# Kernel optimization log

Measured on AMD Instinct MI355X. Metric: run time of the kernel, lower is better.

## Reference

```python
import jax, jax.numpy as jnp
import numpy as np

A_DIM = 18
HID = 512
LSTM_IN = HID + A_DIM + 1  # 531


def setup_inputs() -> dict:
    key = jax.random.key(0)
    ks = jax.random.split(key, 26)
    T, B = 80, 64
    inp = {}
    inp["o"] = jax.random.randint(ks[0], (T, B, 1, 84, 84), 0, 255, dtype=jnp.int32)
    inp["a"] = jax.random.randint(ks[1], (T, B), 0, A_DIM, dtype=jnp.int32)
    inp["r"] = jax.random.normal(ks[2], (T, B), dtype=jnp.float32)
    inp["done"] = jax.random.randint(ks[3], (T, B), 0, 2, dtype=jnp.int32)
    inp["h0"] = jnp.zeros((B, HID), dtype=jnp.float32)
    inp["c0"] = jnp.zeros((B, HID), dtype=jnp.float32)

    def gw(k, shape, s=0.05):
        return (jax.random.normal(k, shape, dtype=jnp.float32) * s)

    # CNN trunk params (torch Conv2d OIHW layout)
    inp["conv1_w"] = gw(ks[4], (32, 1, 8, 8))
    inp["conv1_b"] = jnp.zeros((32,), jnp.float32)
    inp["conv2_w"] = gw(ks[5], (64, 32, 4, 4))
    inp["conv2_b"] = jnp.zeros((64,), jnp.float32)
    inp["conv3_w"] = gw(ks[6], (64, 64, 3, 3))
    inp["conv3_b"] = jnp.zeros((64,), jnp.float32)
    inp["fc_w"] = gw(ks[7], (HID, 64 * 7 * 7))
    inp["fc_b"] = jnp.zeros((HID,), jnp.float32)
    # LSTM params (torch gate order: i, f, g, o)
    inp["W_ih"] = gw(ks[8], (4 * HID, LSTM_IN))
    inp["W_hh"] = gw(ks[9], (4 * HID, HID))
    inp["b_ih"] = jnp.zeros((4 * HID,), jnp.float32)
    inp["b_hh"] = jnp.zeros((4 * HID,), jnp.float32)
    # Dueling heads
    inp["adv_w1"] = gw(ks[10], (HID, HID))
    inp["adv_b1"] = jnp.zeros((HID,), jnp.float32)
    inp["adv_w2"] = gw(ks[11], (A_DIM, HID))
    inp["adv_b2"] = jnp.zeros((A_DIM,), jnp.float32)
    inp["val_w1"] = gw(ks[12], (HID, HID))
    inp["val_b1"] = jnp.zeros((HID,), jnp.float32)
    inp["val_w2"] = gw(ks[13], (1, HID))
    inp["val_b2"] = jnp.zeros((1,), jnp.float32)
    return inp


def _conv(x, w, b, stride):
    y = jax.lax.conv_general_dilated(
        x, w, (stride, stride), 'VALID',
        dimension_numbers=('NCHW', 'OIHW', 'NCHW'))
    return y + b[None, :, None, None]


def reference(o, a, r, done, h0, c0,
              conv1_w, conv1_b, conv2_w, conv2_b, conv3_w, conv3_b,
              fc_w, fc_b, W_ih, W_hh, b_ih, b_hh,
              adv_w1, adv_b1, adv_w2, adv_b2,
              val_w1, val_b1, val_w2, val_b2):
    T, B = o.shape[0], o.shape[1]
    x = o.reshape(T * B, 1, 84, 84).astype(jnp.float32) / 255.0
    x = jax.nn.relu(_conv(x, conv1_w, conv1_b, 4))   # [TB,32,20,20]
    x = jax.nn.relu(_conv(x, conv2_w, conv2_b, 2))   # [TB,64,9,9]
    x = jax.nn.relu(_conv(x, conv3_w, conv3_b, 1))   # [TB,64,7,7]
    x = x.reshape(T * B, 64 * 7 * 7)
    hidden = jax.nn.relu(x @ fc_w.T + fc_b).reshape(T, B, HID)

    a_one_hot = jax.nn.one_hot(a, A_DIM, dtype=jnp.float32)      # [T,B,A]
    lstm_in = jnp.concatenate([hidden, r[..., None], a_one_hot], axis=-1)  # [T,B,531]
    keep = (1.0 - done.astype(jnp.float32))[..., None]           # [T,B,1]
    bias = b_ih + b_hh

    def step(carry, inp_t):
        h, c = carry
        x_t, m = inp_t
        h = h * m
        c = c * m
        g = x_t @ W_ih.T + h @ W_hh.T + bias   # [B, 4H]
        i, f, gg, oo = jnp.split(g, 4, axis=-1)
        c = jax.nn.sigmoid(f) * c + jax.nn.sigmoid(i) * jnp.tanh(gg)
        h = jax.nn.sigmoid(oo) * jnp.tanh(c)
        return (h, c), h

    (hT, cT), hs = jax.lax.scan(step, (h0, c0), (lstm_in, keep))
    z = hs.reshape(T * B, HID)

    adv = jax.nn.relu(z @ adv_w1.T + adv_b1) @ adv_w2.T + adv_b2  # [TB,A]
    val = jax.nn.relu(z @ val_w1.T + val_b1) @ val_w2.T + val_b2  # [TB,1]
    q = val + (adv - adv.mean(axis=1, keepdims=True))
    return q.reshape(T, B, A_DIM), hT, cT
```

## Files before the change

### kernel.cpp

```cpp
#include <hip/hip_runtime.h>
#include <hip/hip_bf16.h>
#include <stdint.h>

typedef __bf16 bf16;
typedef __bf16 bfrag __attribute__((ext_vector_type(8)));
typedef short s16x8 __attribute__((ext_vector_type(8)));
typedef float f32x4 __attribute__((ext_vector_type(4)));
typedef float f32x16 __attribute__((ext_vector_type(16)));
typedef uint32_t u32x4 __attribute__((ext_vector_type(4)));

#define DEV __device__ __forceinline__

DEV bfrag ldg16(const bf16* p){ return *(const bfrag*)p; }

struct U64x2 { uint64_t a, b; };
DEV bfrag ld2x8(const bf16* p){
  U64x2 t; t.a = *(const uint64_t*)p; t.b = *(const uint64_t*)(p+4);
  return __builtin_bit_cast(bfrag, t);
}
DEV bfrag ld4x4(const char* p){
  u32x4 t;
  t[0] = *(const uint32_t*)p;
  t[1] = *(const uint32_t*)(p+4);
  t[2] = *(const uint32_t*)(p+8);
  t[3] = *(const uint32_t*)(p+12);
  return __builtin_bit_cast(bfrag, t);
}

DEV f32x4  mfma16(bfrag a, bfrag b, f32x4  c){ return __builtin_amdgcn_mfma_f32_16x16x32_bf16(a,b,c,0,0,0); }
DEV f32x16 mfma32(bfrag a, bfrag b, f32x16 c){ return __builtin_amdgcn_mfma_f32_32x32x16_bf16(a,b,c,0,0,0); }

DEV f32x16 zero16(){
  f32x16 v;
  for(int i=0;i<16;++i) v[i]=0.f;
  return v;
}
DEV f32x4 zero4(){
  f32x4 v;
  for(int i=0;i<4;++i) v[i]=0.f;
  return v;
}

DEV float sigm(float x){ return 1.0f/(1.0f+__expf(-x)); }
DEV float ftanh(float x){ float e = __expf(2.f*x); return 1.f - 2.f/(e+1.f); }

DEV u32x4 ldcg4(const uint32_t* p){
  u32x4 r;
  asm volatile("global_load_dwordx4 %0, %1, off sc0 sc1" : "=v"(r) : "v"(p));
  return r;
}

DEV uint32_t pk2f(float a, float b){
  bf16 x = (bf16)a, y = (bf16)b;
  return (uint32_t)__builtin_bit_cast(uint16_t,x) | ((uint32_t)__builtin_bit_cast(uint16_t,y)<<16);
}

DEV void gl_lds16(const bf16* g, void* l){
  __builtin_amdgcn_global_load_lds(
      (const __attribute__((address_space(1))) uint32_t*)g,
      (__attribute__((address_space(3))) uint32_t*)l, 16, 0, 0);
}

__global__ __launch_bounds__(256) void k_prep(
    const float* __restrict__ c1w, const float* __restrict__ c2w,
    const float* __restrict__ c3w, const float* __restrict__ fcw,
    const float* __restrict__ Wih, const float* __restrict__ WhhF,
    const float* __restrict__ bih, const float* __restrict__ bhh,
    const float* __restrict__ aw1, const float* __restrict__ aw2,
    const float* __restrict__ vw1, const float* __restrict__ vw2,
    const float* __restrict__ h0, const float* __restrict__ ab1,
    const float* __restrict__ vb1,
    bf16* w1b, bf16* w2r, bf16* w3r, bf16* fcwr, bf16* Wx, bf16* Whh,
    float* biasL, float* Wr, float* Wa, bf16* headw1, float* headb1,
    bf16* w2cat, uint32_t* hcurT)
{
  long i = (long)blockIdx.x*256 + threadIdx.x;
  if (i < 2048){ int co=(int)(i>>6), k=(int)(i&63);
    w1b[i] = (bf16)(c1w[co*64+k]*(1.f/255.f)); return; } i -= 2048;
  if (i < 32768){ int o=(int)(i>>9), k=(int)(i&511);
    int ky=k>>7, kx=(k>>5)&3, ci=k&31;
    w2r[i] = (bf16)c2w[((o*32+ci)*4+ky)*4+kx]; return; } i -= 32768;
  if (i < 36864){ int o=(int)(i/576), k=(int)(i%576);
    int ky=k/192, rem=k-ky*192, kx=rem>>6, ci=rem&63;
    w3r[i] = (bf16)c3w[((o*64+ci)*3+ky)*3+kx]; return; } i -= 36864;
  if (i < 1605632){
    int o=(int)(i/3136), rem=(int)(i%3136);
    int ci=rem/49, yx=rem-ci*49, y=yx/7, x=yx-y*7;
    fcwr[o*3200 + y*448 + x*64 + ci] = (bf16)fcw[i]; return; } i -= 1605632;
  if (i < 32768){ int o=(int)(i>>6), k=(int)(i&63);
    fcwr[o*3200 + 3136 + k] = (bf16)0.f; return; } i -= 32768;
  if (i < 1048576){ int n=(int)(i>>9), k=(int)(i&511);
    Wx[i] = (bf16)Wih[n*531+k]; return; } i -= 1048576;
  if (i < 1048576){ int n=(int)(i>>9), k=(int)(i&511);
    Whh[i] = (bf16)WhhF[n*512+k]; return; } i -= 1048576;
  if (i < 2048){ biasL[i] = bih[i]+bhh[i]; return; } i -= 2048;
  if (i < 2048){ Wr[i] = Wih[i*531+512]; return; } i -= 2048;
  if (i < 36864){ int j=(int)(i>>11), n=(int)(i&2047);
    Wa[i] = Wih[n*531+513+j]; return; } i -= 36864;
  if (i < 524288){ headw1[i] = (bf16)(i<262144 ? aw1[i] : vw1[i-262144]); return; } i -= 524288;
  if (i < 1024){ headb1[i] = (i<512) ? ab1[i] : vb1[i-512]; return; } i -= 1024;
  if (i < 32768){ int n=(int)(i>>10), k=(int)(i&1023);
    float v = 0.f;
    if (n<18 && k<512) v = aw2[n*512+k];
    else if (n==18 && k>=512) v = vw2[k-512];
    w2cat[i] = (bf16)v; return; } i -= 32768;
  if (i < 32768){
    if (i < 16384){
      int row = (int)(i>>8), wd = (int)(i&255);
      uint32_t pk = pk2f(h0[row*512 + wd*2], h0[row*512 + wd*2 + 1]);
      hcurT[i] = pk & ~0x00010001u;
    } else {
      hcurT[i] = 0x00010000u;
    }
    return;
  }
}

__global__ __launch_bounds__(256,2) void k_conv12(
    const int* __restrict__ o, const bf16* __restrict__ w1b,
    const float* __restrict__ c1b, const bf16* __restrict__ w2r,
    const float* __restrict__ c2b, bf16* __restrict__ act2)
{
  __shared__ bf16 lact[2][15200];
  const int tid = threadIdx.x;
  const int w = tid>>6, l = tid&63;
  const int img = w>>1, h = w&1;
  const long gimg = (long)blockIdx.x*2 + img;
  const int* ip = o + gimg*7056;
  char* lw = (char*)&lact[img][0];
  {
    bfrag bw[4];
    #pragma unroll
    for (int ks=0;ks<4;++ks) bw[ks] = ldg16(w1b + (l&31)*64 + ks*16 + 8*(l>>5));
    const float bias = c1b[l&31];
    for (int mt=h; mt<13; mt+=2){
      f32x16 acc = zero16();
      int m0 = mt*32 + (l&31);
      int p  = m0>399 ? 399 : m0;
      int oy = p/20, ox = p - oy*20;
      #pragma unroll
      for (int ks=0;ks<4;++ks){
        int ky = 2*ks + (l>>5);
        const int* q = ip + (oy*4+ky)*84 + ox*4;
        int4 i0 = *(const int4*)q;
        int4 i1 = *(const int4*)(q+4);
        bfrag a;
        a[0]=(bf16)(float)i0.x; a[1]=(bf16)(float)i0.y;
        a[2]=(bf16)(float)i0.z; a[3]=(bf16)(float)i0.w;
        a[4]=(bf16)(float)i1.x; a[5]=(bf16)(float)i1.y;
        a[6]=(bf16)(float)i1.z; a[7]=(bf16)(float)i1.w;
        acc = mfma32(a, bw[ks], acc);
      }
      #pragma unroll
      for (int r2=0;r2<16;++r2){
        int row = (r2&3) + 8*(r2>>2) + 4*(l>>5);
        int m = mt*32 + row;
        if (m < 400){
          float v = acc[r2] + bias; v = v>0.f ? v : 0.f;
          *(bf16*)(lw + m*76 + (l&31)*2) = (bf16)v;
        }
      }
    }
  }
  __syncthreads();
  {
    f32x16 acc2[3];
    #pragma unroll
    for (int a2=0;a2<3;++a2) acc2[a2]=zero16();
    int pb[3];
    #pragma unroll
    for (int mt=0;mt<3;++mt){
      int m = mt*32 + (l&31); int p = m>80 ? 80 : m;
      int oy = p/9, ox = p - oy*9;
      pb[mt] = (oy*2)*20 + ox*2;
    }
    #pragma unroll 4
    for (int ks=0; ks<32; ++ks){
      int k  = ks*16 + 8*(l>>5);
      int ky = k>>7, kx = (k>>5)&3, ci = k&31;
      bfrag b0 = ldg16(w2r + (32*h + (l&31))*512 + k);
      #pragma unroll
      for (int mt=0; mt<3; ++mt){
        int p2 = pb[mt] + ky*20 + kx;
        bfrag a = ld4x4(lw + p2*76 + ci*2);
        acc2[mt] = mfma32(a, b0, acc2[mt]);
      }
    }
    const float bias2 = c2b[32*h + (l&31)];
    #pragma unroll
    for (int mt=0; mt<3; ++mt){
      #pragma unroll
      for (int r2=0;r2<16;++r2){
        int row = (r2&3) + 8*(r2>>2) + 4*(l>>5);
        int m = mt*32 + row;
        if (m < 81){
          float v = acc2[mt][r2] + bias2; v = v>0.f ? v : 0.f;
          act2[gimg*5184 + m*64 + 32*h + (l&31)] = (bf16)v;
        }
      }
    }
  }
}

__global__ __launch_bounds__(256,2) void k_conv3(
    const bf16* __restrict__ act2, const bf16* __restrict__ w3r,
    const float* __restrict__ c3b, bf16* __restrict__ act3)
{
  const int tid=threadIdx.x, w=tid>>6, l=tid&63;
  const long img = (long)blockIdx.x*4 + w;
  const bf16* A = act2 + img*5184;
  f32x16 acc[2][2];
  #pragma unroll
  for(int a2=0;a2<2;++a2){ acc[a2][0]=zero16(); acc[a2][1]=zero16(); }
  #pragma unroll 4
  for (int ks=0; ks<36; ++ks){
    int k  = ks*16 + 8*(l>>5);
    int ky = k/192, rem = k - ky*192, kx = rem>>6, ci = rem&63;
    bfrag b0 = ldg16(w3r + (l&31)*576 + k);
    bfrag b1 = ldg16(w3r + (32+(l&31))*576 + k);
    #pragma unroll
    for (int mt=0; mt<2; ++mt){
      int m = mt*32 + (l&31); int p = m>48 ? 48 : m;
      int oy = p/7, ox = p - oy*7;
      bfrag a = ldg16(A + ((oy+ky)*9 + (ox+kx))*64 + ci);
      acc[mt][0] = mfma32(a, b0, acc[mt][0]);
      acc[mt][1] = mfma32(a, b1, acc[mt][1]);
    }
  }
  const float bias0 = c3b[l&31], bias1 = c3b[32+(l&31)];
  #pragma unroll
  for (int mt=0; mt<2; ++mt){
    #pragma unroll
    for (int r2=0;r2<16;++r2){
      int row = (r2&3) + 8*(r2>>2) + 4*(l>>5);
      int m = mt*32 + row;
      if (m < 50){
        float v0 = 0.f, v1 = 0.f;
        if (m < 49){
          v0 = acc[mt][0][r2] + bias0; v0 = v0>0.f ? v0 : 0.f;
          v1 = acc[mt][1][r2] + bias1; v1 = v1>0.f ? v1 : 0.f;
        }
        act3[img*3200 + m*64 + (l&31)]      = (bf16)v0;
        act3[img*3200 + m*64 + 32 + (l&31)] = (bf16)v1;
      }
    }
  }
}

template<bool RELU, bool OUTBF16>
__global__ __launch_bounds__(256,4) void k_gemm(
    const bf16* __restrict__ A, long lda,
    const bf16* __restrict__ W, long ldb,
    const float* __restrict__ bias,
    float* __restrict__ outF, bf16* __restrict__ outB, long ldo, int K,
    const float* __restrict__ fixR, const int* __restrict__ fixA,
    const float* __restrict__ fixWr, const float* __restrict__ fixWa)
{
  __shared__ bf16 sA[8192];
  char* sb = (char*)sA;
  const int tid=threadIdx.x, w=tid>>6, l=tid&63;
  const int m0 = blockIdx.x*64, n0 = blockIdx.y*128;
  f32x16 acc[2]; acc[0]=zero16(); acc[1]=zero16();
  const int mt = w&1;
  const int rowa = mt*32 + (l&31);
  for (int kc=0; kc<K; kc+=128){
    __syncthreads();
    #pragma unroll
    for (int j=0;j<4;++j){
      int idx = j*64 + l;
      int row = w*16 + (idx>>4);
      int seg = idx&15;
      const bf16* gp = A + (long)(m0+row)*lda + kc + (((seg*16) ^ ((row&15)<<4))>>1);
      gl_lds16(gp, sb + w*4096 + j*1024);
    }
    asm volatile("s_waitcnt vmcnt(0)" ::: "memory");
    __syncthreads();
    #pragma unroll
    for (int ks=0; ks<8; ++ks){
      bfrag a = *(const bfrag*)(sb + rowa*256 + ((ks*32 + (l>>5)*16) ^ ((rowa&15)<<4)));
      #pragma unroll
      for (int j=0;j<2;++j){
        int nt = (w>>1)*2 + j;
        bfrag b = ldg16(W + (long)(n0 + nt*32 + (l&31))*ldb + kc + ks*16 + 8*(l>>5));
        acc[j] = mfma32(a, b, acc[j]);
      }
    }
  }
  #pragma unroll
  for (int j=0;j<2;++j){
    int nt = (w>>1)*2 + j;
    int gc = n0 + nt*32 + (l&31);
    float bv = bias ? bias[gc] : 0.f;
    float wrv = fixR ? fixWr[gc] : 0.f;
    #pragma unroll
    for (int r2=0;r2<16;++r2){
      int row = (r2&3) + 8*(r2>>2) + 4*(l>>5);
      long gr = m0 + mt*32 + row;
      float v = acc[j][r2] + bv;
      if (fixR) v += fixR[gr]*wrv + fixWa[(long)fixA[gr]*2048 + gc];
      if (RELU) v = v>0.f ? v : 0.f;
      if (OUTBF16) outB[gr*ldo + gc] = (bf16)v;
      else         outF[gr*ldo + gc] = v;
    }
  }
}

__global__ __launch_bounds__(256,1) void k_lstm(
    const bf16* __restrict__ G, const int* __restrict__ done,
    const float* __restrict__ c0, const bf16* __restrict__ Whh,
    uint32_t* __restrict__ hcurT, bf16* __restrict__ hseq,
    float* __restrict__ outH, float* __restrict__ outC)
{
  __shared__ bf16 sh2[8192];
  __shared__ float sg[4][16][33];
  __shared__ float sc[16][33];
  __shared__ char  sdone[80][16];
  const int tid=threadIdx.x, w=tid>>6, l=tid&63;
  const int blk=blockIdx.x;
  const int grp=(blk&7)>>1, jj=((blk&1)<<3)|(blk>>3);
  const int bb = grp*16, uu = jj*32;

  for (int p=tid; p<512; p+=256){ int m=p>>5, u=p&31; sc[m][u] = c0[(bb+m)*512 + uu + u]; }
  for (int p=tid; p<1280; p+=256){ int t=p>>4, m=p&15; sdone[t][m] = (char)done[t*64 + bb + m]; }

  bfrag wb0[16], wb1[16];
  {
    const long row0 = (long)w*512 + uu + (l&15);
    #pragma unroll
    for (int ks=0; ks<16; ++ks){
      int k = ks*32 + 8*(l>>4);
      wb0[ks] = ldg16(Whh + row0*512 + k);
      wb1[ks] = ldg16(Whh + (row0+16)*512 + k);
      asm volatile("" : "+v"(wb0[ks]), "+v"(wb1[ks]));
    }
  }

  char* shb = (char*)sh2;
  const int loff = l*16;
  const int srow  = tid>>4;
  const int sci   = tid&15;

  __syncthreads();

  for (int t=0; t<80; ++t){
    float gv0[4], gv1[4];
    {
      const bf16* Gt = G + ((long)t*64 + bb)*2048 + w*512 + uu;
      #pragma unroll
      for (int r2=0;r2<4;++r2){
        int m2 = (l>>4)*4 + r2;
        gv0[r2] = (float)Gt[(long)m2*2048 + (l&15)];
        gv1[r2] = (float)Gt[(long)m2*2048 + 16 + (l&15)];
      }
    }
    __builtin_amdgcn_sched_barrier(0);
    {
      const uint32_t* hb = hcurT + (size_t)(t&1)*16384 + (size_t)(bb+srow)*256 + sci*16;
      u32x4 hv[4];
      const uint32_t expPat = ((uint32_t)(t&1)) | (((uint32_t)((t>>1)&1))<<16);
      for (;;){
        #pragma unroll
        for (int j2=0;j2<4;++j2) hv[j2] = ldcg4(hb + j2*4);
        asm volatile("s_waitcnt vmcnt(0)" ::: "memory");
        bool ok = true;
        #pragma unroll
        for (int j2=0;j2<4;++j2){
          ok &= ((hv[j2][0]&0x00010001u)==expPat) & ((hv[j2][1]&0x00010001u)==expPat)
              & ((hv[j2][2]&0x00010001u)==expPat) & ((hv[j2][3]&0x00010001u)==expPat);
        }
        if (__all(ok)) break;
        __builtin_amdgcn_s_sleep(1);
      }
      if (sdone[t][srow]){
        #pragma unroll
        for (int j2=0;j2<4;++j2){ u32x4 z = {0,0,0,0}; hv[j2] = z; }
      } else {
        #pragma unroll
        for (int j2=0;j2<4;++j2){
          hv[j2][0] &= ~0x00010001u; hv[j2][1] &= ~0x00010001u;
          hv[j2][2] &= ~0x00010001u; hv[j2][3] &= ~0x00010001u;
        }
      }
      #pragma unroll
      for (int j=0;j<4;++j){
        *(u32x4*)(shb + sci*1024 + ((((srow + 16*j)*16)) ^ ((sci&7)<<4))) = hv[j];
      }
    }
    __syncthreads();
    f32x4 a0e = zero4(), a0o = zero4(), a1e = zero4(), a1o = zero4();
    #pragma unroll
    for (int ks=0; ks<16; ++ks){
      bfrag a = *(const bfrag*)(shb + ks*1024 + (loff ^ ((ks&7)<<4)));
      if (ks & 1){ a0o = mfma16(a, wb0[ks], a0o); a1o = mfma16(a, wb1[ks], a1o); }
      else       { a0e = mfma16(a, wb0[ks], a0e); a1e = mfma16(a, wb1[ks], a1e); }
    }
    #pragma unroll
    for (int r2=0;r2<4;++r2){
      int m = (l>>4)*4 + r2;
      sg[w][m][(l&15)]    = a0e[r2] + a0o[r2] + gv0[r2];
      sg[w][m][16+(l&15)] = a1e[r2] + a1o[r2] + gv1[r2];
    }
    __syncthreads();
    {
      int p0 = tid*2; int m = p0>>5, u = p0&31;
      int dn = sdone[t][m];
      float c_0 = dn ? 0.f : sc[m][u];
      float c_1 = dn ? 0.f : sc[m][u+1];
      float i0=sg[0][m][u],   f0=sg[1][m][u],   g0=sg[2][m][u],   o0=sg[3][m][u];
      float i1=sg[0][m][u+1], f1=sg[1][m][u+1], g1=sg[2][m][u+1], o1=sg[3][m][u+1];
      float cn0 = sigm(f0)*c_0 + sigm(i0)*ftanh(g0);
      float cn1 = sigm(f1)*c_1 + sigm(i1)*ftanh(g1);
      float h_0 = sigm(o0)*ftanh(cn0);
      float h_1 = sigm(o1)*ftanh(cn1);
      sc[m][u] = cn0; sc[m][u+1] = cn1;
      uint32_t pk = pk2f(h_0, h_1);
      int p1 = (t+1)&3;
      uint32_t pat = ((uint32_t)(p1&1)) | (((uint32_t)(p1>>1))<<16);
      uint32_t pkT = (pk & ~0x00010001u) | pat;
      __hip_atomic_store(
          hcurT + (size_t)((t+1)&1)*16384 + (size_t)(bb+m)*256 + ((uu+u)>>1),
          pkT, __ATOMIC_RELAXED, __HIP_MEMORY_SCOPE_AGENT);
      *(uint32_t*)(hseq + ((long)t*64 + bb + m)*512 + uu + u) = pk;
      if (t == 79){
        outH[(bb+m)*512 + uu + u]   = h_0;  outH[(bb+m)*512 + uu + u+1] = h_1;
        outC[(bb+m)*512 + uu + u]   = cn0;  outC[(bb+m)*512 + uu + u+1] = cn1;
      }
    }
  }
}

__global__ __launch_bounds__(256) void k_qhead(
    const bf16* __restrict__ zav, const bf16* __restrict__ w2cat,
    const float* __restrict__ ab2, const float* __restrict__ vb2,
    float* __restrict__ q)
{
  __shared__ float sq[4][16][33];
  const int tid=threadIdx.x, w=tid>>6, l=tid&63;
  const int s0 = blockIdx.x*64 + w*16;
  f32x4 acc0 = zero4(), acc1 = zero4();
  const int row = l&15;
  #pragma unroll 4
  for (int ks=0; ks<32; ++ks){
    int k = ks*32 + 8*(l>>4);
    bfrag a  = ldg16(zav + (long)(s0+row)*1024 + k);
    bfrag b0 = ldg16(w2cat + (l&15)*1024 + k);
    bfrag b1 = ldg16(w2cat + (16+(l&15))*1024 + k);
    acc0 = mfma16(a, b0, acc0);
    acc1 = mfma16(a, b1, acc1);
  }
  #pragma unroll
  for (int r2=0;r2<4;++r2){
    int m = (l>>4)*4 + r2;
    sq[w][m][l&15]      = acc0[r2];
    sq[w][m][16+(l&15)] = acc1[r2];
  }
  __syncthreads();
  if (l < 16){
    int s = s0 + l;
    float av[18]; float sum = 0.f;
    #pragma unroll
    for (int j=0;j<18;++j){ av[j] = sq[w][l][j] + ab2[j]; sum += av[j]; }
    float val = sq[w][l][18] + vb2[0];
    float mean = sum * (1.f/18.f);
    #pragma unroll
    for (int j=0;j<18;++j) q[(long)s*18 + j] = val + av[j] - mean;
  }
}

extern "C" void kernel_launch(void* const* d_in, const int* in_sizes, int n_in,
                              void* d_out, int out_size, void* d_ws, size_t ws_size,
                              hipStream_t stream)
{
  (void)in_sizes; (void)n_in; (void)out_size;
  const int*   o_in = (const int*)  d_in[0];
  const int*   a_in = (const int*)  d_in[1];
  const float* r_in = (const float*)d_in[2];
  const int*   done = (const int*)  d_in[3];
  const float* h0   = (const float*)d_in[4];
  const float* c0   = (const float*)d_in[5];
  const float* c1w  = (const float*)d_in[6],  *c1b=(const float*)d_in[7];
  const float* c2w  = (const float*)d_in[8],  *c2b=(const float*)d_in[9];
  const float* c3w  = (const float*)d_in[10], *c3b=(const float*)d_in[11];
  const float* fcw  = (const float*)d_in[12], *fcb=(const float*)d_in[13];
  const float* Wih  = (const float*)d_in[14], *WhhF=(const float*)d_in[15];
  const float* bih  = (const float*)d_in[16], *bhh=(const float*)d_in[17];
  const float* aw1  = (const float*)d_in[18], *ab1=(const float*)d_in[19];
  const float* aw2  = (const float*)d_in[20], *ab2=(const float*)d_in[21];
  const float* vw1  = (const float*)d_in[22], *vb1=(const float*)d_in[23];
  const float* vw2  = (const float*)d_in[24], *vb2=(const float*)d_in[25];

  char* ws = (char*)d_ws;
  size_t off = 0;
  auto alloc = [&](size_t b){ size_t p = off; off = (off + b + 255) & ~(size_t)255; return p; };
  bf16*  act2   = (bf16*) (ws + alloc(53084160));
  bf16*  act3   = (bf16*) (ws + alloc(32768000));
  bf16*  hidden = (bf16*) (ws + alloc(5242880));
  uint32_t* hcurT = (uint32_t*)(ws + alloc(131072));
  bf16*  w1b    = (bf16*) (ws + alloc(4096));
  bf16*  w2r    = (bf16*) (ws + alloc(65536));
  bf16*  w3r    = (bf16*) (ws + alloc(73728));
  bf16*  fcwr   = (bf16*) (ws + alloc(3276800));
  bf16*  Wx     = (bf16*) (ws + alloc(2097152));
  bf16*  Whh    = (bf16*) (ws + alloc(2097152));
  float* biasL  = (float*)(ws + alloc(8192));
  float* Wr     = (float*)(ws + alloc(8192));
  float* Wa     = (float*)(ws + alloc(147456));
  bf16*  headw1 = (bf16*) (ws + alloc(1048576));
  float* headb1 = (float*)(ws + alloc(4096));
  bf16*  w2cat  = (bf16*) (ws + alloc(65536));
  if (off > ws_size) return;

  bf16*  G    = act2;
  bf16*  hseq = hidden;
  bf16*  zav  = act3;

  float* qout = (float*)d_out;
  float* outH = qout + 92160;
  float* outC = qout + 124928;

  k_prep<<<17340, 256, 0, stream>>>(c1w, c2w, c3w, fcw, Wih, WhhF, bih, bhh,
      aw1, aw2, vw1, vw2, h0, ab1, vb1, w1b, w2r, w3r, fcwr, Wx, Whh,
      biasL, Wr, Wa, headw1, headb1, w2cat, hcurT);

  k_conv12<<<2560, 256, 0, stream>>>(o_in, w1b, c1b, w2r, c2b, act2);
  k_conv3<<<1280, 256, 0, stream>>>(act2, w3r, c3b, act3);
  k_gemm<true,true><<<dim3(80,4), 256, 0, stream>>>(
      act3, 3200, fcwr, 3200, fcb, nullptr, hidden, 512, 3200,
      nullptr, nullptr, nullptr, nullptr);
  k_gemm<false,true><<<dim3(80,16), 256, 0, stream>>>(
      hidden, 512, Wx, 512, biasL, nullptr, G, 2048, 512,
      r_in, a_in, Wr, Wa);

  k_lstm<<<64, 256, 0, stream>>>(G, done, c0, Whh, hcurT, hseq, outH, outC);

  k_gemm<true,true><<<dim3(80,8), 256, 0, stream>>>(
      hseq, 512, headw1, 512, headb1, nullptr, zav, 1024, 512,
      nullptr, nullptr, nullptr, nullptr);
  k_qhead<<<80, 256, 0, stream>>>(zav, w2cat, ab2, vb2, qout);
}
```

Before: 604.2 us.

## Split conv12 across four waves per image with register-resident conv2 weights

The conv1+conv2 kernel now launches 512 threads, so each image is handled by four waves instead of two. The conv1 row tiles are spread over four waves. Conv2 switches from 32x32 MFMA tiles over 32-channel halves to 16x16x32 MFMA tiles over 16-column quarters. Each wave preloads all 16 of its conv2 weight fragments into registers once, instead of reloading a weight fragment from global memory every k-step. This aims to raise parallelism per image and remove repeated weight loads, at the cost of more VGPRs and a larger block that could limit occupancy.

Result: slower. 706.9 us (+17.0%).

```diff
diff --git a/kernel.cpp b/kernel.cpp
--- a/kernel.cpp
+++ b/kernel.cpp
@@ -116,7 +116,7 @@
   }
 }
 
-__global__ __launch_bounds__(256,2) void k_conv12(
+__global__ __launch_bounds__(512,2) void k_conv12(
     const int* __restrict__ o, const bf16* __restrict__ w1b,
     const float* __restrict__ c1b, const bf16* __restrict__ w2r,
     const float* __restrict__ c2b, bf16* __restrict__ act2)
@@ -124,7 +124,7 @@
   __shared__ bf16 lact[2][15200];
   const int tid = threadIdx.x;
   const int w = tid>>6, l = tid&63;
-  const int img = w>>1, h = w&1;
+  const int img = w>>2, q = w&3;
   const long gimg = (long)blockIdx.x*2 + img;
   const int* ip = o + gimg*7056;
   char* lw = (char*)&lact[img][0];
@@ -133,7 +133,7 @@
     #pragma unroll
     for (int ks=0;ks<4;++ks) bw[ks] = ldg16(w1b + (l&31)*64 + ks*16 + 8*(l>>5));
     const float bias = c1b[l&31];
-    for (int mt=h; mt<13; mt+=2){
+    for (int mt=q; mt<13; mt+=4){
       f32x16 acc = zero16();
       int m0 = mt*32 + (l&31);
       int p  = m0>399 ? 399 : m0;
@@ -141,9 +141,9 @@
       #pragma unroll
       for (int ks=0;ks<4;++ks){
         int ky = 2*ks + (l>>5);
-        const int* q = ip + (oy*4+ky)*84 + ox*4;
-        int4 i0 = *(const int4*)q;
-        int4 i1 = *(const int4*)(q+4);
+        const int* qq = ip + (oy*4+ky)*84 + ox*4;
+        int4 i0 = *(const int4*)qq;
+        int4 i1 = *(const int4*)(qq+4);
         bfrag a;
         a[0]=(bf16)(float)i0.x; a[1]=(bf16)(float)i0.y;
         a[2]=(bf16)(float)i0.z; a[3]=(bf16)(float)i0.w;
@@ -164,38 +164,39 @@
   }
   __syncthreads();
   {
-    f32x16 acc2[3];
-    #pragma unroll
-    for (int a2=0;a2<3;++a2) acc2[a2]=zero16();
-    int pb[3];
-    #pragma unroll
-    for (int mt=0;mt<3;++mt){
-      int m = mt*32 + (l&31); int p = m>80 ? 80 : m;
+    const int col = q*16 + (l&15);
+    bfrag wb[16];
+    #pragma unroll
+    for (int ks=0;ks<16;++ks) wb[ks] = ldg16(w2r + (long)col*512 + ks*32 + 8*(l>>4));
+    int pbase[6];
+    #pragma unroll
+    for (int rt=0;rt<6;++rt){
+      int m = rt*16 + (l&15); int p = m>80 ? 80 : m;
       int oy = p/9, ox = p - oy*9;
-      pb[mt] = (oy*2)*20 + ox*2;
-    }
+      pbase[rt] = ((oy*2)*20 + ox*2)*76 + 16*(l>>4);
+    }
+    f32x4 acc[6];
+    #pragma unroll
+    for (int rt=0;rt<6;++rt) acc[rt] = zero4();
     #pragma unroll 4
-    for (int ks=0; ks<32; ++ks){
-      int k  = ks*16 + 8*(l>>5);
-      int ky = k>>7, kx = (k>>5)&3, ci = k&31;
-      bfrag b0 = ldg16(w2r + (32*h + (l&31))*512 + k);
-      #pragma unroll
-      for (int mt=0; mt<3; ++mt){
-        int p2 = pb[mt] + ky*20 + kx;
-        bfrag a = ld4x4(lw + p2*76 + ci*2);
-        acc2[mt] = mfma32(a, b0, acc2[mt]);
-      }
-    }
-    const float bias2 = c2b[32*h + (l&31)];
-    #pragma unroll
-    for (int mt=0; mt<3; ++mt){
-      #pragma unroll
-      for (int r2=0;r2<16;++r2){
-        int row = (r2&3) + 8*(r2>>2) + 4*(l>>5);
-        int m = mt*32 + row;
+    for (int ks=0; ks<16; ++ks){
+      int ky = ks>>2, kx = ks&3;
+      int koff = (ky*20 + kx)*76;
+      #pragma unroll
+      for (int rt=0;rt<6;++rt){
+        bfrag a = ld4x4(lw + pbase[rt] + koff);
+        acc[rt] = mfma16(a, wb[ks], acc[rt]);
+      }
+    }
+    const float bias2 = c2b[col];
+    #pragma unroll
+    for (int rt=0;rt<6;++rt){
+      #pragma unroll
+      for (int r2=0;r2<4;++r2){
+        int m = rt*16 + (l>>4)*4 + r2;
         if (m < 81){
-          float v = acc2[mt][r2] + bias2; v = v>0.f ? v : 0.f;
-          act2[gimg*5184 + m*64 + 32*h + (l&31)] = (bf16)v;
+          float v = acc[rt][r2] + bias2; v = v>0.f ? v : 0.f;
+          act2[gimg*5184 + m*64 + col] = (bf16)v;
         }
       }
     }
@@ -522,7 +523,7 @@
       aw1, aw2, vw1, vw2, h0, ab1, vb1, w1b, w2r, w3r, fcwr, Wx, Whh,
       biasL, Wr, Wa, headw1, headb1, w2cat, hcurT);
 
-  k_conv12<<<2560, 256, 0, stream>>>(o_in, w1b, c1b, w2r, c2b, act2);
+  k_conv12<<<2560, 512, 0, stream>>>(o_in, w1b, c1b, w2r, c2b, act2);
   k_conv3<<<1280, 256, 0, stream>>>(act2, w3r, c3b, act3);
   k_gemm<true,true><<<dim3(80,4), 256, 0, stream>>>(
       act3, 3200, fcwr, 3200, fcb, nullptr, hidden, 512, 3200,
```
